# Optimization experiments

Measured on AMD Instinct MI355X. Metric: run time of the kernel, lower is better.

The kernel has to match this reference:

```python
import jax, jax.numpy as jnp
import numpy as np

D = 512
H = 8
DV = D // H  # 64
NEG_INF = -1e30


def setup_inputs() -> dict:
    key = jax.random.key(0)
    ks = jax.random.split(key, 10)
    B, S = 4, 2048
    x = jax.random.normal(ks[0], (B, D, S), dtype=jnp.float32)
    mask = jnp.ones((B, S), dtype=jnp.float32)
    s = 1.0 / np.sqrt(D)
    sv = 1.0 / np.sqrt(D)
    # per-head Linear(d -> dv) weights stacked: [H, dv, d] (torch Linear layout W @ x)
    Wq = jax.random.uniform(ks[1], (H, DV, D), jnp.float32, -s, s)
    bq = jax.random.uniform(ks[2], (H, DV), jnp.float32, -s, s)
    Wk = jax.random.uniform(ks[3], (H, DV, D), jnp.float32, -s, s)
    bk = jax.random.uniform(ks[4], (H, DV), jnp.float32, -s, s)
    Wv = jax.random.uniform(ks[5], (H, DV, D), jnp.float32, -s, s)
    bv = jax.random.uniform(ks[6], (H, DV), jnp.float32, -s, s)
    W0 = jax.random.uniform(ks[7], (D, D), jnp.float32, -sv, sv)
    b0 = jax.random.uniform(ks[8], (D,), jnp.float32, -sv, sv)
    return {"x": x, "mask": mask, "Wq": Wq, "bq": bq, "Wk": Wk, "bk": bk,
            "Wv": Wv, "bv": bv, "W0": W0, "b0": b0}


def reference(x, mask, Wq, bq, Wk, bk, Wv, bv, W0, b0):
    # x: [B, d, S] -> xt: [B, S, d]
    xt = jnp.transpose(x, (0, 2, 1))
    # fused per-head projections: [B, H, S, dv]
    q = jnp.einsum('bsd,hed->bhse', xt, Wq) + bq[None, :, None, :]
    k = jnp.einsum('bsd,hed->bhse', xt, Wk) + bk[None, :, None, :]
    v = jnp.einsum('bsd,hed->bhse', xt, Wv) + bv[None, :, None, :]
    dv = q.shape[-1]
    scores = jnp.einsum('bhse,bhte->bhst', q, k) * (1.0 / np.sqrt(dv))
    # mask_logits (QANet style): keep where mask==1, else -1e30; mask over key dim
    h_mask = mask[:, None, None, :]  # [B,1,1,S]
    scores = scores * h_mask + (1.0 - h_mask) * NEG_INF
    p = jax.nn.softmax(scores, axis=-1)
    # zero out fully-masked query rows via v_mask on query dim
    p = p * mask[:, None, :, None]
    out = jnp.einsum('bhst,bhte->bhse', p, v)  # [B,H,S,dv]
    # concat heads along feature dim -> [B, S, d]
    B, _, S, _ = out.shape
    heads = jnp.transpose(out, (0, 2, 1, 3)).reshape(B, S, -1)
    y = heads @ W0.T + b0  # output projection
    return jnp.transpose(y, (0, 2, 1))  # [B, d, S]
```

## Files before the change

### kernel.cpp

```cpp
#include <hip/hip_runtime.h>

#define B_  4
#define D_  512
#define H_  8
#define DV_ 64
#define S_  2048

typedef __bf16 bf16;
typedef bf16  bf16x8 __attribute__((ext_vector_type(8)));
typedef bf16  bf16x4 __attribute__((ext_vector_type(4)));
typedef float f32x4  __attribute__((ext_vector_type(4)));

#define MFMA(a, b, c) __builtin_amdgcn_mfma_f32_16x16x32_bf16((a), (b), (c), 0, 0, 0)

#define GLOAD_LDS(g, l)                                                     \
    __builtin_amdgcn_global_load_lds(                                       \
        (const __attribute__((address_space(1))) void*)(g),                 \
        (__attribute__((address_space(3))) void*)(l), 16, 0, 0)

#define WAIT_VMCNT(n)                                                       \
    __builtin_amdgcn_s_waitcnt(((n) & 15) | (((n) >> 4) << 14) | (7 << 4) | (15 << 8))

__global__ __launch_bounds__(256) void prep(
    const float* __restrict__ x, const float* __restrict__ Wq,
    const float* __restrict__ Wk, const float* __restrict__ Wv,
    const float* __restrict__ W0, bf16* __restrict__ xb, bf16* __restrict__ Wb) {
    const int bid = blockIdx.x;
    if (bid < 4096) {
        __shared__ float tile[32][33];
        const int sblk = bid % 64;
        const int dblk = (bid / 64) % 16;
        const int b    = bid / 1024;
        const int d0 = dblk * 32, s0 = sblk * 32;
        const int tx = threadIdx.x & 31;
        const int ty = threadIdx.x >> 5;
        const float* xp = x + (size_t)b * D_ * S_;
#pragma unroll
        for (int i = 0; i < 32; i += 8)
            tile[ty + i][tx] = xp[(size_t)(d0 + ty + i) * S_ + s0 + tx];
        __syncthreads();
        bf16* xbp = xb + ((size_t)b * S_ + s0) * D_ + d0;
#pragma unroll
        for (int i = 0; i < 32; i += 8)
            xbp[(size_t)(ty + i) * D_ + tx] = (bf16)tile[tx][ty + i];
    } else {
        const int f0 = ((bid - 4096) * 256 + threadIdx.x) * 16;
        const int src = f0 >> 18;
        const int off = f0 & 262143;
        const float* W = (src == 0) ? Wq : (src == 1) ? Wk : (src == 2) ? Wv : W0;
        float4 v0 = *(const float4*)&W[off];
        float4 v1 = *(const float4*)&W[off + 4];
        float4 v2 = *(const float4*)&W[off + 8];
        float4 v3 = *(const float4*)&W[off + 12];
        bf16x8 h0 = {(bf16)v0.x, (bf16)v0.y, (bf16)v0.z, (bf16)v0.w,
                     (bf16)v1.x, (bf16)v1.y, (bf16)v1.z, (bf16)v1.w};
        bf16x8 h1 = {(bf16)v2.x, (bf16)v2.y, (bf16)v2.z, (bf16)v2.w,
                     (bf16)v3.x, (bf16)v3.y, (bf16)v3.z, (bf16)v3.w};
        *(bf16x8*)&Wb[f0]     = h0;
        *(bf16x8*)&Wb[f0 + 8] = h1;
    }
}

__global__ __launch_bounds__(256) void gemm_qkv(
    const bf16* __restrict__ A, const bf16* __restrict__ Wb,
    const float* __restrict__ bq, const float* __restrict__ bk,
    const float* __restrict__ bv,
    bf16* __restrict__ Q, bf16* __restrict__ K, bf16* __restrict__ Vt) {
    __shared__ union {
        struct { bf16 A[8192]; bf16 B[8192]; } s;
        bf16 T[128][132];
    } sm;

    const int tid = threadIdx.x;
    const int w = tid >> 6, lane = tid & 63;
    const int m16 = lane & 15, quad = lane >> 4;
    const int wr = w & 1, wc = w >> 1;

    const int nblk = blockIdx.x % 12;
    const int mblk = blockIdx.x / 12;
    const int m0 = mblk * 128, n0 = nblk * 128;

    f32x4 acc[4][4];
#pragma unroll
    for (int i = 0; i < 4; ++i)
#pragma unroll
        for (int j = 0; j < 4; ++j) acc[i][j] = (f32x4){0.f, 0.f, 0.f, 0.f};

    for (int k0 = 0; k0 < D_; k0 += 64) {
        __syncthreads();
#pragma unroll
        for (int i = 0; i < 4; ++i) {
            const int c  = w * 4 + i;
            const int mt = c >> 1, kk = c & 1;
            const int row = mt * 16 + m16;
            const int col = k0 + kk * 32 + quad * 8;
            GLOAD_LDS(&A[(size_t)(m0 + row) * D_ + col],  &sm.s.A[(c * 64 + lane) * 8]);
            GLOAD_LDS(&Wb[(size_t)(n0 + row) * D_ + col], &sm.s.B[(c * 64 + lane) * 8]);
        }
        __syncthreads();
#pragma unroll
        for (int kk = 0; kk < 2; ++kk) {
            bf16x8 af[4], bfv[4];
#pragma unroll
            for (int t = 0; t < 4; ++t) {
                af[t]  = *(const bf16x8*)&sm.s.A[(((wr * 4 + t) * 2 + kk) * 64 + lane) * 8];
                bfv[t] = *(const bf16x8*)&sm.s.B[(((wc * 4 + t) * 2 + kk) * 64 + lane) * 8];
            }
#pragma unroll
            for (int mt = 0; mt < 4; ++mt)
#pragma unroll
                for (int nt = 0; nt < 4; ++nt)
                    acc[mt][nt] = MFMA(af[mt], bfv[nt], acc[mt][nt]);
        }
    }

    const int proj = n0 >> 9;
    const float* bias = (proj == 0) ? bq : (proj == 1) ? bk : bv;

    if (proj == 2) {
#pragma unroll
        for (int mt = 0; mt < 4; ++mt)
#pragma unroll
            for (int nt = 0; nt < 4; ++nt) {
                const int nr = (n0 + wc * 64 + nt * 16 + m16) & 511;
                const int h = nr >> 6, e = nr & 63;
                const float bia = bias[nr];
                const int srow = m0 + wr * 64 + mt * 16 + quad * 4;
                const int b = srow >> 11, s = srow & 2047;
                const int s2 = (s & ~31) | (quad * 8 + (mt & 1) * 4);
                bf16x4 hv;
#pragma unroll
                for (int r = 0; r < 4; ++r) hv[r] = (bf16)(acc[mt][nt][r] + bia);
                *(bf16x4*)&Vt[(((size_t)b * H_ + h) * DV_ + e) * S_ + s2] = hv;
            }
    } else {
        __syncthreads();
#pragma unroll
        for (int mt = 0; mt < 4; ++mt)
#pragma unroll
            for (int nt = 0; nt < 4; ++nt) {
                const int nloc = wc * 64 + nt * 16 + m16;
                const float bia = bias[(n0 + nloc) & 511];
#pragma unroll
                for (int r = 0; r < 4; ++r)
                    sm.T[wr * 64 + mt * 16 + quad * 4 + r][nloc] =
                        (bf16)(acc[mt][nt][r] + bia);
            }
        __syncthreads();
        const int rloc = tid >> 1, cb = (tid & 1) * 64;
        const int M = m0 + rloc, b = M >> 11, s = M & 2047;
        const int nrb = (n0 + cb) & 511;
        const int h = nrb >> 6;
        bf16* dst = ((proj == 0) ? Q : K) + (((size_t)b * H_ + h) * S_ + s) * DV_;
#pragma unroll
        for (int u = 0; u < 8; ++u)
            *(bf16x8*)&dst[u * 8] = *(const bf16x8*)&sm.T[rloc][cb + u * 8];
    }
}

__global__ __launch_bounds__(256, 2) void flash_attn(
    const bf16* __restrict__ Q, const bf16* __restrict__ K, const bf16* __restrict__ Vt,
    const float* __restrict__ mask, bf16* __restrict__ heads) {
    __shared__ union {
        struct {
            bf16 Kl[2][4][2048];
            bf16 Vl[2][4][2048];
            float Ms[2048];
        } s;
        struct { float O[64][65]; float L[64]; } red;
    } sm;

    const int bid  = blockIdx.x;
    const int bidx = (bid & 7) * 128 + (bid >> 3);
    const int qblk = bidx & 31;
    const int h    = (bidx >> 5) & 7;
    const int b    = bidx >> 8;
    const int q0   = qblk * 64;

    const int tid = threadIdx.x;
    const int w = tid >> 6, lane = tid & 63;
    const int m16 = lane & 15, quad = lane >> 4;

    const bf16* Qp = Q  + ((size_t)b * H_ + h) * S_ * DV_;
    const bf16* Kp = K  + ((size_t)b * H_ + h) * S_ * DV_;
    const bf16* Vp = Vt + ((size_t)b * H_ + h) * DV_ * S_;
    const float* mp = mask + (size_t)b * S_;

    const int krow = lane >> 3;
    const int kcol = ((lane & 7) ^ krow) * 8;
    const int vrow = lane >> 2;
    const int vcol = ((lane & 3) ^ (vrow & 3)) * 8;

    bf16x8 qf[4][2];
#pragma unroll
    for (int qt = 0; qt < 4; ++qt)
#pragma unroll
        for (int kk = 0; kk < 2; ++kk) {
            bf16x8 v = *(const bf16x8*)&Qp[(size_t)(q0 + qt * 16 + m16) * DV_ +
                                           kk * 32 + quad * 8];
#pragma unroll
            for (int i = 0; i < 8; ++i) v[i] = (bf16)((float)v[i] * 0.125f);
            qf[qt][kk] = v;
        }

    bf16x8 ones;
#pragma unroll
    for (int i = 0; i < 8; ++i) ones[i] = (bf16)1.0f;

    f32x4 o[4][4];
    f32x4 lacc[4];
#pragma unroll
    for (int mt = 0; mt < 4; ++mt)
#pragma unroll
        for (int qt = 0; qt < 4; ++qt) o[mt][qt] = (f32x4){0.f, 0.f, 0.f, 0.f};
#pragma unroll
    for (int qt = 0; qt < 4; ++qt) lacc[qt] = (f32x4){0.f, 0.f, 0.f, 0.f};

#pragma unroll
    for (int p = 0; p < 2; ++p)
        GLOAD_LDS(&mp[(p * 256 + tid) * 4], &sm.s.Ms[(p * 256 + tid) * 4]);
    {
        const int tw = w * 32;
#pragma unroll
        for (int p = 0; p < 4; ++p)
            GLOAD_LDS(&Kp[(size_t)(tw + p * 8 + krow) * DV_ + kcol],
                      &sm.s.Kl[0][w][(p * 64 + lane) * 8]);
#pragma unroll
        for (int p = 0; p < 4; ++p)
            GLOAD_LDS(&Vp[(size_t)(p * 16 + vrow) * S_ + tw + vcol],
                      &sm.s.Vl[0][w][(p * 64 + lane) * 8]);
    }
    __syncthreads();

    for (int i = 0; i < 16; ++i) {
        const int tw = i * 128 + w * 32;
        if (i < 15) {
            const int twn = tw + 128;
            const int nb = (i + 1) & 1;
#pragma unroll
            for (int p = 0; p < 4; ++p)
                GLOAD_LDS(&Kp[(size_t)(twn + p * 8 + krow) * DV_ + kcol],
                          &sm.s.Kl[nb][w][(p * 64 + lane) * 8]);
#pragma unroll
            for (int p = 0; p < 4; ++p)
                GLOAD_LDS(&Vp[(size_t)(p * 16 + vrow) * S_ + twn + vcol],
                          &sm.s.Vl[nb][w][(p * 64 + lane) * 8]);
            WAIT_VMCNT(8);
        } else {
            WAIT_VMCNT(0);
        }
        const int buf = i & 1;

        bf16x8 kf[2][2];
#pragma unroll
        for (int tt = 0; tt < 2; ++tt)
#pragma unroll
            for (int kk = 0; kk < 2; ++kk)
                kf[tt][kk] = *(const bf16x8*)&sm.s.Kl[buf][w][
                    ((tt * 16 + m16) * 8 + ((kk * 4 + quad) ^ (m16 & 7))) * 8];
        bf16x8 vf[4];
#pragma unroll
        for (int mt = 0; mt < 4; ++mt)
            vf[mt] = *(const bf16x8*)&sm.s.Vl[buf][w][
                ((mt * 16 + m16) * 4 + (quad ^ (m16 & 3))) * 8];
        const f32x4 mq0 = *(const f32x4*)&sm.s.Ms[tw + quad * 4];
        const f32x4 mq1 = *(const f32x4*)&sm.s.Ms[tw + 16 + quad * 4];

        f32x4 sc[2][4];
#pragma unroll
        for (int tt = 0; tt < 2; ++tt)
#pragma unroll
            for (int qt = 0; qt < 4; ++qt) sc[tt][qt] = (f32x4){0.f, 0.f, 0.f, 0.f};
#pragma unroll
        for (int kk = 0; kk < 2; ++kk)
#pragma unroll
            for (int tt = 0; tt < 2; ++tt)
#pragma unroll
                for (int qt = 0; qt < 4; ++qt)
                    sc[tt][qt] = MFMA(kf[tt][kk], qf[qt][kk], sc[tt][qt]);

        f32x4 ng0, ng1;
#pragma unroll
        for (int r = 0; r < 4; ++r) {
            ng0[r] = (1.0f - mq0[r]) * -1e30f;
            ng1[r] = (1.0f - mq1[r]) * -1e30f;
        }
        bf16x8 pf[4];
#pragma unroll
        for (int qt = 0; qt < 4; ++qt)
#pragma unroll
            for (int r = 0; r < 4; ++r) {
                pf[qt][r]     = (bf16)__expf(sc[0][qt][r] * mq0[r] + ng0[r]);
                pf[qt][4 + r] = (bf16)__expf(sc[1][qt][r] * mq1[r] + ng1[r]);
            }

#pragma unroll
        for (int mt = 0; mt < 4; ++mt)
#pragma unroll
            for (int qt = 0; qt < 4; ++qt) o[mt][qt] = MFMA(vf[mt], pf[qt], o[mt][qt]);
#pragma unroll
        for (int qt = 0; qt < 4; ++qt) lacc[qt] = MFMA(ones, pf[qt], lacc[qt]);
    }

    __syncthreads();
#pragma unroll
    for (int ww = 0; ww < 4; ++ww) {
        if (w == ww) {
#pragma unroll
            for (int mt = 0; mt < 4; ++mt)
#pragma unroll
                for (int qt = 0; qt < 4; ++qt)
#pragma unroll
                    for (int r = 0; r < 4; ++r) {
                        float* slot = &sm.red.O[mt * 16 + quad * 4 + r][qt * 16 + m16];
                        *slot = (ww == 0) ? o[mt][qt][r] : (*slot + o[mt][qt][r]);
                    }
            if (quad == 0)
#pragma unroll
                for (int qt = 0; qt < 4; ++qt) {
                    float* ls = &sm.red.L[qt * 16 + m16];
                    *ls = (ww == 0) ? lacc[qt][0] : (*ls + lacc[qt][0]);
                }
        }
        __syncthreads();
    }

    const int ql = tid >> 2, ec = (tid & 3) * 16;
    const float l  = sm.red.L[ql];
    const float qm = mp[q0 + ql];
    const float inv = qm / l;
    bf16x8 hv[2];
#pragma unroll
    for (int c = 0; c < 2; ++c)
#pragma unroll
        for (int i = 0; i < 8; ++i)
            hv[c][i] = (bf16)(sm.red.O[ec + c * 8 + i][ql] * inv);
    bf16* dst = &heads[((size_t)b * S_ + q0 + ql) * D_ + h * DV_ + ec];
    *(bf16x8*)(dst)     = hv[0];
    *(bf16x8*)(dst + 8) = hv[1];
}

__global__ __launch_bounds__(256) void gemm_out(
    const bf16* __restrict__ A, const bf16* __restrict__ Wb,
    const float* __restrict__ b0, float* __restrict__ outp) {
    __shared__ bf16 Asl[8192];
    __shared__ bf16 Bsl[8192];

    const int tid = threadIdx.x;
    const int w = tid >> 6, lane = tid & 63;
    const int m16 = lane & 15, quad = lane >> 4;
    const int wr = w & 1, wc = w >> 1;

    const int nblk = blockIdx.x & 3;
    const int mblk = blockIdx.x >> 2;
    const int m0 = mblk * 128, n0 = nblk * 128;

    f32x4 acc[4][4];
#pragma unroll
    for (int i = 0; i < 4; ++i)
#pragma unroll
        for (int j = 0; j < 4; ++j) acc[i][j] = (f32x4){0.f, 0.f, 0.f, 0.f};

    for (int k0 = 0; k0 < D_; k0 += 64) {
        __syncthreads();
#pragma unroll
        for (int i = 0; i < 4; ++i) {
            const int c  = w * 4 + i;
            const int mt = c >> 1, kk = c & 1;
            const int row = mt * 16 + m16;
            const int col = k0 + kk * 32 + quad * 8;
            GLOAD_LDS(&A[(size_t)(m0 + row) * D_ + col], &Asl[(c * 64 + lane) * 8]);
            GLOAD_LDS(&Wb[(size_t)(1536 + n0 + row) * D_ + col], &Bsl[(c * 64 + lane) * 8]);
        }
        __syncthreads();
#pragma unroll
        for (int kk = 0; kk < 2; ++kk) {
            bf16x8 af[4], bfv[4];
#pragma unroll
            for (int t = 0; t < 4; ++t) {
                af[t]  = *(const bf16x8*)&Asl[(((wr * 4 + t) * 2 + kk) * 64 + lane) * 8];
                bfv[t] = *(const bf16x8*)&Bsl[(((wc * 4 + t) * 2 + kk) * 64 + lane) * 8];
            }
#pragma unroll
            for (int mt = 0; mt < 4; ++mt)
#pragma unroll
                for (int nt = 0; nt < 4; ++nt)
                    acc[mt][nt] = MFMA(af[mt], bfv[nt], acc[mt][nt]);
        }
    }

#pragma unroll
    for (int mt = 0; mt < 4; ++mt)
#pragma unroll
        for (int nt = 0; nt < 4; ++nt) {
            const int n = n0 + wc * 64 + nt * 16 + m16;
            const float bia = b0[n];
            const int srow = m0 + wr * 64 + mt * 16 + quad * 4;
            const int b = srow >> 11, s = srow & 2047;
            float4 vv;
            vv.x = acc[mt][nt][0] + bia;
            vv.y = acc[mt][nt][1] + bia;
            vv.z = acc[mt][nt][2] + bia;
            vv.w = acc[mt][nt][3] + bia;
            *(float4*)&outp[((size_t)b * D_ + n) * S_ + s] = vv;
        }
}

extern "C" void kernel_launch(void* const* d_in, const int* in_sizes, int n_in,
                              void* d_out, int out_size, void* d_ws, size_t ws_size,
                              hipStream_t stream) {
    const float* x    = (const float*)d_in[0];
    const float* mask = (const float*)d_in[1];
    const float* Wq   = (const float*)d_in[2];
    const float* bq   = (const float*)d_in[3];
    const float* Wk   = (const float*)d_in[4];
    const float* bk   = (const float*)d_in[5];
    const float* Wv   = (const float*)d_in[6];
    const float* bv   = (const float*)d_in[7];
    const float* W0   = (const float*)d_in[8];
    const float* b0   = (const float*)d_in[9];
    float* out = (float*)d_out;

    char* ws = (char*)d_ws;
    const size_t SEG = (size_t)B_ * S_ * D_ * sizeof(bf16);
    bf16* xb    = (bf16*)(ws);
    bf16* Qb    = (bf16*)(ws + SEG);
    bf16* Kb    = (bf16*)(ws + 2 * SEG);
    bf16* Vt    = (bf16*)(ws + 3 * SEG);
    bf16* Wb    = (bf16*)(ws + 4 * SEG);
    bf16* heads = xb;

    prep<<<dim3(4096 + 256), dim3(256), 0, stream>>>(x, Wq, Wk, Wv, W0, xb, Wb);
    gemm_qkv<<<dim3(64 * 12), dim3(256), 0, stream>>>(xb, Wb, bq, bk, bv, Qb, Kb, Vt);
    flash_attn<<<dim3(B_ * H_ * (S_ / 64)), dim3(256), 0, stream>>>(Qb, Kb, Vt, mask, heads);
    gemm_out<<<dim3(64 * 4), dim3(256), 0, stream>>>(heads, Wb, b0, out);
}
```

Before: 201.2 us.

## Load K/V fragments directly from global into registers, drop LDS staging

Replaces the double-buffered global_load_lds staging of K and V tiles with direct global-to-register fragment loads. K fragments are software-pipelined one iteration ahead via two register sets, and V is loaded inside each compute step. The mask is pre-scaled by log2(e) so the exponent uses the native exp2 builtin in a single fma. This removes LDS traffic and the vmcnt waits, but exposes global-load latency for V, which is no longer prefetched, and uses more registers.

```diff
diff --git a/kernel.cpp b/kernel.cpp
--- a/kernel.cpp
+++ b/kernel.cpp
@@ -5,6 +5,7 @@
 #define H_  8
 #define DV_ 64
 #define S_  2048
+#define LOG2E 1.442695041f
 
 typedef __bf16 bf16;
 typedef bf16  bf16x8 __attribute__((ext_vector_type(8)));
@@ -17,9 +18,6 @@
     __builtin_amdgcn_global_load_lds(                                       \
         (const __attribute__((address_space(1))) void*)(g),                 \
         (__attribute__((address_space(3))) void*)(l), 16, 0, 0)
-
-#define WAIT_VMCNT(n)                                                       \
-    __builtin_amdgcn_s_waitcnt(((n) & 15) | (((n) >> 4) << 14) | (7 << 4) | (15 << 8))
 
 __global__ __launch_bounds__(256) void prep(
     const float* __restrict__ x, const float* __restrict__ Wq,
@@ -158,15 +156,70 @@
     }
 }
 
+#define LOADK(DST, TW)                                                       \
+    {                                                                        \
+        _Pragma("unroll")                                                    \
+        for (int tt = 0; tt < 2; ++tt)                                       \
+            _Pragma("unroll")                                                \
+            for (int kk = 0; kk < 2; ++kk)                                   \
+                DST[tt][kk] = *(const bf16x8*)&Kp[                           \
+                    (size_t)((TW) + tt * 16 + m16) * DV_ + kk * 32 + quad * 8]; \
+    }
+
+#define COMPUTE(TW, KF)                                                      \
+    {                                                                        \
+        const int tw_ = (TW);                                                \
+        bf16x8 vfr[4];                                                       \
+        _Pragma("unroll")                                                    \
+        for (int mt = 0; mt < 4; ++mt)                                       \
+            vfr[mt] = *(const bf16x8*)&Vp[(size_t)(mt * 16 + m16) * S_ +     \
+                                          tw_ + quad * 8];                   \
+        const f32x4 m2a = *(const f32x4*)&sm.Ms[tw_ + quad * 4];             \
+        const f32x4 m2b = *(const f32x4*)&sm.Ms[tw_ + 16 + quad * 4];        \
+        f32x4 sc[2][4];                                                      \
+        _Pragma("unroll")                                                    \
+        for (int tt = 0; tt < 2; ++tt)                                       \
+            _Pragma("unroll")                                                \
+            for (int qt = 0; qt < 4; ++qt)                                   \
+                sc[tt][qt] = (f32x4){0.f, 0.f, 0.f, 0.f};                    \
+        _Pragma("unroll")                                                    \
+        for (int kk = 0; kk < 2; ++kk)                                       \
+            _Pragma("unroll")                                                \
+            for (int tt = 0; tt < 2; ++tt)                                   \
+                _Pragma("unroll")                                            \
+                for (int qt = 0; qt < 4; ++qt)                               \
+                    sc[tt][qt] = MFMA(KF[tt][kk], qf[qt][kk], sc[tt][qt]);   \
+        f32x4 ngA, ngB;                                                      \
+        _Pragma("unroll")                                                    \
+        for (int r = 0; r < 4; ++r) {                                        \
+            ngA[r] = (m2a[r] - LOG2E) * 8e29f;                               \
+            ngB[r] = (m2b[r] - LOG2E) * 8e29f;                               \
+        }                                                                    \
+        bf16x8 pf[4];                                                        \
+        _Pragma("unroll")                                                    \
+        for (int qt = 0; qt < 4; ++qt)                                       \
+            _Pragma("unroll")                                                \
+            for (int r = 0; r < 4; ++r) {                                    \
+                pf[qt][r] = (bf16)__builtin_amdgcn_exp2f(                    \
+                    __builtin_fmaf(sc[0][qt][r], m2a[r], ngA[r]));           \
+                pf[qt][4 + r] = (bf16)__builtin_amdgcn_exp2f(                \
+                    __builtin_fmaf(sc[1][qt][r], m2b[r], ngB[r]));           \
+            }                                                                \
+        _Pragma("unroll")                                                    \
+        for (int mt = 0; mt < 4; ++mt)                                       \
+            _Pragma("unroll")                                                \
+            for (int qt = 0; qt < 4; ++qt)                                   \
+                o[mt][qt] = MFMA(vfr[mt], pf[qt], o[mt][qt]);                \
+        _Pragma("unroll")                                                    \
+        for (int qt = 0; qt < 4; ++qt)                                       \
+            lacc[qt] = MFMA(ones, pf[qt], lacc[qt]);                         \
+    }
+
 __global__ __launch_bounds__(256, 2) void flash_attn(
     const bf16* __restrict__ Q, const bf16* __restrict__ K, const bf16* __restrict__ Vt,
     const float* __restrict__ mask, bf16* __restrict__ heads) {
     __shared__ union {
-        struct {
-            bf16 Kl[2][4][2048];
-            bf16 Vl[2][4][2048];
-            float Ms[2048];
-        } s;
+        float Ms[2048];
         struct { float O[64][65]; float L[64]; } red;
     } sm;
 
@@ -186,10 +239,12 @@
     const bf16* Vp = Vt + ((size_t)b * H_ + h) * DV_ * S_;
     const float* mp = mask + (size_t)b * S_;
 
-    const int krow = lane >> 3;
-    const int kcol = ((lane & 7) ^ krow) * 8;
-    const int vrow = lane >> 2;
-    const int vcol = ((lane & 3) ^ (vrow & 3)) * 8;
+#pragma unroll
+    for (int p = 0; p < 2; ++p) {
+        const float4 mv = *(const float4*)&mp[(p * 256 + tid) * 4];
+        f32x4 t = {mv.x * LOG2E, mv.y * LOG2E, mv.z * LOG2E, mv.w * LOG2E};
+        *(f32x4*)&sm.Ms[(p * 256 + tid) * 4] = t;
+    }
 
     bf16x8 qf[4][2];
 #pragma unroll
@@ -216,90 +271,15 @@
 #pragma unroll
     for (int qt = 0; qt < 4; ++qt) lacc[qt] = (f32x4){0.f, 0.f, 0.f, 0.f};
 
-#pragma unroll
-    for (int p = 0; p < 2; ++p)
-        GLOAD_LDS(&mp[(p * 256 + tid) * 4], &sm.s.Ms[(p * 256 + tid) * 4]);
-    {
-        const int tw = w * 32;
-#pragma unroll
-        for (int p = 0; p < 4; ++p)
-            GLOAD_LDS(&Kp[(size_t)(tw + p * 8 + krow) * DV_ + kcol],
-                      &sm.s.Kl[0][w][(p * 64 + lane) * 8]);
-#pragma unroll
-        for (int p = 0; p < 4; ++p)
-            GLOAD_LDS(&Vp[(size_t)(p * 16 + vrow) * S_ + tw + vcol],
-                      &sm.s.Vl[0][w][(p * 64 + lane) * 8]);
-    }
+    bf16x8 kfA[2][2], kfB[2][2];
+    LOADK(kfA, w * 32);
     __syncthreads();
 
-    for (int i = 0; i < 16; ++i) {
-        const int tw = i * 128 + w * 32;
-        if (i < 15) {
-            const int twn = tw + 128;
-            const int nb = (i + 1) & 1;
-#pragma unroll
-            for (int p = 0; p < 4; ++p)
-                GLOAD_LDS(&Kp[(size_t)(twn + p * 8 + krow) * DV_ + kcol],
-                          &sm.s.Kl[nb][w][(p * 64 + lane) * 8]);
-#pragma unroll
-            for (int p = 0; p < 4; ++p)
-                GLOAD_LDS(&Vp[(size_t)(p * 16 + vrow) * S_ + twn + vcol],
-                          &sm.s.Vl[nb][w][(p * 64 + lane) * 8]);
-            WAIT_VMCNT(8);
-        } else {
-            WAIT_VMCNT(0);
-        }
-        const int buf = i & 1;
-
-        bf16x8 kf[2][2];
-#pragma unroll
-        for (int tt = 0; tt < 2; ++tt)
-#pragma unroll
-            for (int kk = 0; kk < 2; ++kk)
-                kf[tt][kk] = *(const bf16x8*)&sm.s.Kl[buf][w][
-                    ((tt * 16 + m16) * 8 + ((kk * 4 + quad) ^ (m16 & 7))) * 8];
-        bf16x8 vf[4];
-#pragma unroll
-        for (int mt = 0; mt < 4; ++mt)
-            vf[mt] = *(const bf16x8*)&sm.s.Vl[buf][w][
-                ((mt * 16 + m16) * 4 + (quad ^ (m16 & 3))) * 8];
-        const f32x4 mq0 = *(const f32x4*)&sm.s.Ms[tw + quad * 4];
-        const f32x4 mq1 = *(const f32x4*)&sm.s.Ms[tw + 16 + quad * 4];
-
-        f32x4 sc[2][4];
-#pragma unroll
-        for (int tt = 0; tt < 2; ++tt)
-#pragma unroll
-            for (int qt = 0; qt < 4; ++qt) sc[tt][qt] = (f32x4){0.f, 0.f, 0.f, 0.f};
-#pragma unroll
-        for (int kk = 0; kk < 2; ++kk)
-#pragma unroll
-            for (int tt = 0; tt < 2; ++tt)
-#pragma unroll
-                for (int qt = 0; qt < 4; ++qt)
-                    sc[tt][qt] = MFMA(kf[tt][kk], qf[qt][kk], sc[tt][qt]);
-
-        f32x4 ng0, ng1;
-#pragma unroll
-        for (int r = 0; r < 4; ++r) {
-            ng0[r] = (1.0f - mq0[r]) * -1e30f;
-            ng1[r] = (1.0f - mq1[r]) * -1e30f;
-        }
-        bf16x8 pf[4];
-#pragma unroll
-        for (int qt = 0; qt < 4; ++qt)
-#pragma unroll
-            for (int r = 0; r < 4; ++r) {
-                pf[qt][r]     = (bf16)__expf(sc[0][qt][r] * mq0[r] + ng0[r]);
-                pf[qt][4 + r] = (bf16)__expf(sc[1][qt][r] * mq1[r] + ng1[r]);
-            }
-
-#pragma unroll
-        for (int mt = 0; mt < 4; ++mt)
-#pragma unroll
-            for (int qt = 0; qt < 4; ++qt) o[mt][qt] = MFMA(vf[mt], pf[qt], o[mt][qt]);
-#pragma unroll
-        for (int qt = 0; qt < 4; ++qt) lacc[qt] = MFMA(ones, pf[qt], lacc[qt]);
+    for (int i = 0; i < 16; i += 2) {
+        LOADK(kfB, (i + 1) * 128 + w * 32);
+        COMPUTE(i * 128 + w * 32, kfA);
+        if (i < 14) LOADK(kfA, (i + 2) * 128 + w * 32);
+        COMPUTE((i + 1) * 128 + w * 32, kfB);
     }
 
     __syncthreads();
```

Result: slower. 210.0 us (+4.3%).

## Split K/V waits, use exp2 with prescaled mask, and remap GEMM block order

Applied to the files above, without the earlier changes.

The attention loop now waits only for the K tile before computing scores and softmax, and waits for the V tile just before the PV MFMAs. This lets the V load overlap with the QK and exp work. The mask is loaded through registers and prescaled by log2(e) so the kernel can call the native exp2 instead of __expf. Both GEMMs remap block indices with an XCD-style swizzle (blockIdx&7) to improve L2 locality across the chiplets. The vmcnt counts and sched_barriers must match the number of outstanding loads exactly, or the kernel could read stale LDS data.

```diff
diff --git a/kernel.cpp b/kernel.cpp
--- a/kernel.cpp
+++ b/kernel.cpp
@@ -5,6 +5,7 @@
 #define H_  8
 #define DV_ 64
 #define S_  2048
+#define LOG2E 1.442695041f
 
 typedef __bf16 bf16;
 typedef bf16  bf16x8 __attribute__((ext_vector_type(8)));
@@ -76,8 +77,9 @@
     const int m16 = lane & 15, quad = lane >> 4;
     const int wr = w & 1, wc = w >> 1;
 
-    const int nblk = blockIdx.x % 12;
-    const int mblk = blockIdx.x / 12;
+    const int bid  = (blockIdx.x & 7) * 96 + (blockIdx.x >> 3);
+    const int nblk = bid % 12;
+    const int mblk = bid / 12;
     const int m0 = mblk * 128, n0 = nblk * 128;
 
     f32x4 acc[4][4];
@@ -191,6 +193,13 @@
     const int vrow = lane >> 2;
     const int vcol = ((lane & 3) ^ (vrow & 3)) * 8;
 
+#pragma unroll
+    for (int p = 0; p < 2; ++p) {
+        const float4 mv = *(const float4*)&mp[(p * 256 + tid) * 4];
+        f32x4 t = {mv.x * LOG2E, mv.y * LOG2E, mv.z * LOG2E, mv.w * LOG2E};
+        *(f32x4*)&sm.s.Ms[(p * 256 + tid) * 4] = t;
+    }
+
     bf16x8 qf[4][2];
 #pragma unroll
     for (int qt = 0; qt < 4; ++qt)
@@ -216,9 +225,6 @@
 #pragma unroll
     for (int qt = 0; qt < 4; ++qt) lacc[qt] = (f32x4){0.f, 0.f, 0.f, 0.f};
 
-#pragma unroll
-    for (int p = 0; p < 2; ++p)
-        GLOAD_LDS(&mp[(p * 256 + tid) * 4], &sm.s.Ms[(p * 256 + tid) * 4]);
     {
         const int tw = w * 32;
 #pragma unroll
@@ -245,10 +251,11 @@
             for (int p = 0; p < 4; ++p)
                 GLOAD_LDS(&Vp[(size_t)(p * 16 + vrow) * S_ + twn + vcol],
                           &sm.s.Vl[nb][w][(p * 64 + lane) * 8]);
-            WAIT_VMCNT(8);
+            WAIT_VMCNT(12);
         } else {
-            WAIT_VMCNT(0);
-        }
+            WAIT_VMCNT(4);
+        }
+        __builtin_amdgcn_sched_barrier(0);
         const int buf = i & 1;
 
         bf16x8 kf[2][2];
@@ -258,48 +265,56 @@
             for (int kk = 0; kk < 2; ++kk)
                 kf[tt][kk] = *(const bf16x8*)&sm.s.Kl[buf][w][
                     ((tt * 16 + m16) * 8 + ((kk * 4 + quad) ^ (m16 & 7))) * 8];
+        const f32x4 m2a = *(const f32x4*)&sm.s.Ms[tw + quad * 4];
+        const f32x4 m2b = *(const f32x4*)&sm.s.Ms[tw + 16 + quad * 4];
+
+        f32x4 sc[2][4];
+#pragma unroll
+        for (int tt = 0; tt < 2; ++tt)
+#pragma unroll
+            for (int qt = 0; qt < 4; ++qt) sc[tt][qt] = (f32x4){0.f, 0.f, 0.f, 0.f};
+#pragma unroll
+        for (int kk = 0; kk < 2; ++kk)
+#pragma unroll
+            for (int tt = 0; tt < 2; ++tt)
+#pragma unroll
+                for (int qt = 0; qt < 4; ++qt)
+                    sc[tt][qt] = MFMA(kf[tt][kk], qf[qt][kk], sc[tt][qt]);
+
+        f32x4 ngA, ngB;
+#pragma unroll
+        for (int r = 0; r < 4; ++r) {
+            ngA[r] = (m2a[r] - LOG2E) * 8e29f;
+            ngB[r] = (m2b[r] - LOG2E) * 8e29f;
+        }
+        bf16x8 pf[4];
+#pragma unroll
+        for (int qt = 0; qt < 4; ++qt)
+#pragma unroll
+            for (int r = 0; r < 4; ++r) {
+                pf[qt][r]     = (bf16)__builtin_amdgcn_exp2f(
+                    __builtin_fmaf(sc[0][qt][r], m2a[r], ngA[r]));
+                pf[qt][4 + r] = (bf16)__builtin_amdgcn_exp2f(
+                    __builtin_fmaf(sc[1][qt][r], m2b[r], ngB[r]));
+            }
+
+#pragma unroll
+        for (int qt = 0; qt < 4; ++qt) lacc[qt] = MFMA(ones, pf[qt], lacc[qt]);
+
+        if (i < 15) WAIT_VMCNT(8);
+        else        WAIT_VMCNT(0);
+        __builtin_amdgcn_sched_barrier(0);
+
         bf16x8 vf[4];
 #pragma unroll
         for (int mt = 0; mt < 4; ++mt)
             vf[mt] = *(const bf16x8*)&sm.s.Vl[buf][w][
                 ((mt * 16 + m16) * 4 + (quad ^ (m16 & 3))) * 8];
-        const f32x4 mq0 = *(const f32x4*)&sm.s.Ms[tw + quad * 4];
-        const f32x4 mq1 = *(const f32x4*)&sm.s.Ms[tw + 16 + quad * 4];
-
-        f32x4 sc[2][4];
-#pragma unroll
-        for (int tt = 0; tt < 2; ++tt)
-#pragma unroll
-            for (int qt = 0; qt < 4; ++qt) sc[tt][qt] = (f32x4){0.f, 0.f, 0.f, 0.f};
-#pragma unroll
-        for (int kk = 0; kk < 2; ++kk)
-#pragma unroll
-            for (int tt = 0; tt < 2; ++tt)
-#pragma unroll
-                for (int qt = 0; qt < 4; ++qt)
-                    sc[tt][qt] = MFMA(kf[tt][kk], qf[qt][kk], sc[tt][qt]);
-
-        f32x4 ng0, ng1;
-#pragma unroll
-        for (int r = 0; r < 4; ++r) {
-            ng0[r] = (1.0f - mq0[r]) * -1e30f;
-            ng1[r] = (1.0f - mq1[r]) * -1e30f;
-        }
-        bf16x8 pf[4];
-#pragma unroll
-        for (int qt = 0; qt < 4; ++qt)
-#pragma unroll
-            for (int r = 0; r < 4; ++r) {
-                pf[qt][r]     = (bf16)__expf(sc[0][qt][r] * mq0[r] + ng0[r]);
-                pf[qt][4 + r] = (bf16)__expf(sc[1][qt][r] * mq1[r] + ng1[r]);
-            }
 
 #pragma unroll
         for (int mt = 0; mt < 4; ++mt)
 #pragma unroll
             for (int qt = 0; qt < 4; ++qt) o[mt][qt] = MFMA(vf[mt], pf[qt], o[mt][qt]);
-#pragma unroll
-        for (int qt = 0; qt < 4; ++qt) lacc[qt] = MFMA(ones, pf[qt], lacc[qt]);
     }
 
     __syncthreads();
@@ -351,8 +366,9 @@
     const int m16 = lane & 15, quad = lane >> 4;
     const int wr = w & 1, wc = w >> 1;
 
-    const int nblk = blockIdx.x & 3;
-    const int mblk = blockIdx.x >> 2;
+    const int bid  = (blockIdx.x & 7) * 32 + (blockIdx.x >> 3);
+    const int nblk = bid & 3;
+    const int mblk = bid >> 2;
     const int m0 = mblk * 128, n0 = nblk * 128;
 
     f32x4 acc[4][4];
```

After: 196.9 us. 2.1% less time.
